# Kernel optimization log

Measured on AMD Instinct MI355X. Metric: run time of the kernel, lower is better.

Reference implementation:

```python
import jax, jax.numpy as jnp
import numpy as np

E = 16      # num experts
K = 2       # top-k
EPS = np.finfo(float).eps


def setup_inputs() -> dict:
    key = jax.random.key(0)
    k1, k2, k3 = jax.random.split(key, 3)
    B, D_IN, D_OUT = 16384, 1024, 512
    x = jax.random.normal(k1, (B, D_IN), dtype=jnp.float32)
    w_router = jax.random.normal(k2, (D_IN, E), dtype=jnp.float32) * 0.02
    w_experts = jax.random.normal(k3, (E, D_IN, D_OUT), dtype=jnp.float32) * 0.02
    return {"x": x, "w_router": w_router, "w_experts": w_experts}


def reference(x, w_router, w_experts):
    # --- noisy_top_k_gating (eval path: clean logits, no noise) ---
    logits = x @ w_router                      # [B, E]
    top_vals, top_idx = jax.lax.top_k(logits, K)   # [B, K]
    top_gates = jax.nn.softmax(top_vals, axis=1)   # softmax over top-k logits
    B = x.shape[0]
    gates = jnp.zeros_like(logits).at[jnp.arange(B)[:, None], top_idx].set(top_gates)  # [B, E]

    # --- per-expert encode (dense form; zero gates null out non-dispatched pairs,
    #     matching SparseDispatcher's sparse dispatch/combine math exactly) ---
    expert_out = jnp.einsum('bd,edh->beh', x, w_experts)  # [B, E, d_out]

    # --- SparseDispatcher.combine: exp -> gate-weight -> index_add -> eps clamp -> log ---
    combined = jnp.einsum('be,beh->bh', gates, jnp.exp(expert_out))  # [B, d_out]
    combined = jnp.where(combined == 0, jnp.asarray(EPS, combined.dtype), combined)
    return jnp.log(combined)
```

## Files before the change

kernel.cpp:

```cpp
#include <hip/hip_runtime.h>
#include <hip/hip_bf16.h>

typedef unsigned short u16_t;
typedef unsigned int   u32_t;

#define B_ROWS  16384
#define D_IN    1024
#define D_OUT   512
#define NEXP    16
#define CNT_STRIDE 16
#define EPSF    2.2204460492503131e-16f

using short8  = __attribute__((ext_vector_type(8))) short;
using floatx4 = __attribute__((ext_vector_type(4))) float;

__device__ __forceinline__ u16_t f2bf(float f) {
    u32_t u = __float_as_uint(f);
    u += 0x7fffu + ((u >> 16) & 1u);
    return (u16_t)(u >> 16);
}

__global__ __launch_bounds__(256) void transpose_wr(
        const float* __restrict__ wr, float* __restrict__ wrT) {
    int i = blockIdx.x * 256 + threadIdx.x;
    int e = i >> 10, d = i & 1023;
    wrT[i] = wr[d * NEXP + e];
}

__global__ __launch_bounds__(256) void convert_x(
        const float* __restrict__ x, u16_t* __restrict__ xb) {
    size_t i = ((size_t)blockIdx.x * 256 + threadIdx.x) * 8;
    float4 a = *(const float4*)(x + i);
    float4 b = *(const float4*)(x + i + 4);
    union { u16_t us[8]; uint4 v; } p;
    p.us[0] = f2bf(a.x); p.us[1] = f2bf(a.y); p.us[2] = f2bf(a.z); p.us[3] = f2bf(a.w);
    p.us[4] = f2bf(b.x); p.us[5] = f2bf(b.y); p.us[6] = f2bf(b.z); p.us[7] = f2bf(b.w);
    *(uint4*)(xb + i) = p.v;
}

__global__ __launch_bounds__(256) void convert_wT(
        const float* __restrict__ w, u16_t* __restrict__ wT) {
    int b = blockIdx.x;
    int e  = b >> 8;
    int k0 = ((b >> 1) & 127) * 8;
    int n  = (b & 1) * 256 + threadIdx.x;
    const float* src = w + ((size_t)e * D_IN + k0) * D_OUT + n;
    union { u16_t us[8]; uint4 v; } p;
    #pragma unroll
    for (int j = 0; j < 8; ++j) p.us[j] = f2bf(src[(size_t)j * D_OUT]);
    *(uint4*)(wT + ((size_t)e * D_OUT + n) * D_IN + k0) = p.v;
}

__global__ __launch_bounds__(256) void router_kernel(
        const float* __restrict__ x, const float* __restrict__ wrT,
        int* __restrict__ counts, int* __restrict__ rowlist,
        float* __restrict__ gatelist) {
    __shared__ float wsh[NEXP * D_IN];
    __shared__ int hist[NEXP], base[NEXP], hist2[NEXP];
    __shared__ unsigned char eidx_sh[32][2];
    __shared__ float g_sh[32][2];

    int t = threadIdx.x;
    {
        const float4* src = (const float4*)wrT;
        float4* dst = (float4*)wsh;
        #pragma unroll
        for (int i = 0; i < 16; ++i) dst[t + 256 * i] = src[t + 256 * i];
    }
    if (t < NEXP) { hist[t] = 0; hist2[t] = 0; }
    __syncthreads();

    int lr = t >> 3, q = t & 7;
    int row = blockIdx.x * 32 + lr;
    const float4* xq = (const float4*)(x + (size_t)row * D_IN + q * 128);

    double acc[NEXP];
    #pragma unroll
    for (int e = 0; e < NEXP; ++e) acc[e] = 0.0;

    for (int i = 0; i < 32; ++i) {
        int ii = (i + q * 4) & 31;
        float4 xv = xq[ii];
        double x0 = xv.x, x1 = xv.y, x2 = xv.z, x3 = xv.w;
        int d = q * 128 + ii * 4;
        #pragma unroll
        for (int e = 0; e < NEXP; ++e) {
            float4 wv = *(const float4*)(&wsh[e * D_IN + d]);
            acc[e] += x0 * (double)wv.x;
            acc[e] += x1 * (double)wv.y;
            acc[e] += x2 * (double)wv.z;
            acc[e] += x3 * (double)wv.w;
        }
    }
    #pragma unroll
    for (int e = 0; e < NEXP; ++e) {
        acc[e] += __shfl_xor(acc[e], 1);
        acc[e] += __shfl_xor(acc[e], 2);
        acc[e] += __shfl_xor(acc[e], 4);
    }
    if (q == 0) {
        int i1 = 0; double v1 = acc[0];
        #pragma unroll
        for (int e = 1; e < NEXP; ++e) if (acc[e] > v1) { v1 = acc[e]; i1 = e; }
        int i2 = -1; double v2 = -1.0e300;
        #pragma unroll
        for (int e = 0; e < NEXP; ++e) if (e != i1 && acc[e] > v2) { v2 = acc[e]; i2 = e; }
        double ed = exp(v2 - v1);
        double s = 1.0 + ed;
        eidx_sh[lr][0] = (unsigned char)i1; g_sh[lr][0] = (float)(1.0 / s);
        eidx_sh[lr][1] = (unsigned char)i2; g_sh[lr][1] = (float)(ed / s);
        atomicAdd(&hist[i1], 1);
        atomicAdd(&hist[i2], 1);
    }
    __syncthreads();
    if (t < NEXP) base[t] = atomicAdd(&counts[t * CNT_STRIDE], hist[t]);
    __syncthreads();
    if (t < 64) {
        int r = t >> 1, sl = t & 1;
        int e = eidx_sh[r][sl];
        int pos = base[e] + atomicAdd(&hist2[e], 1);
        rowlist[e * B_ROWS + pos] = ((blockIdx.x * 32 + r) << 1) | sl;
        gatelist[e * B_ROWS + pos] = g_sh[r][sl];
    }
}

template<bool USE_CONTRIB>
__global__ __launch_bounds__(256) void moe_gemm_bf16(
        const u16_t* __restrict__ xb, const u16_t* __restrict__ wT,
        const int* __restrict__ counts, const int* __restrict__ rowlist,
        const float* __restrict__ gatelist,
        float* __restrict__ out, float* __restrict__ contrib) {
    int e = blockIdx.z;
    int n_e = counts[e * CNT_STRIDE];
    int ty = blockIdx.y;
    if (ty * 128 >= n_e) return;
    int n0 = blockIdx.x * 128;

    __shared__ u16_t Ash[128][40];
    __shared__ u16_t Bsh[128][40];
    __shared__ int   rid_sh[128];
    __shared__ float gt_sh[128];

    int t = threadIdx.x;
    if (t < 128) {
        int gi = ty * 128 + t;
        int v = 0; float g = 0.f;
        if (gi < n_e) { v = rowlist[e * B_ROWS + gi]; g = gatelist[e * B_ROWS + gi]; }
        rid_sh[t] = v; gt_sh[t] = g;
    }
    __syncthreads();

    int hr = t >> 1, hh = t & 1;
    const u16_t* aptr = xb + (size_t)(rid_sh[hr] >> 1) * D_IN + hh * 16;
    const u16_t* bptr = wT + ((size_t)e * D_OUT + n0 + hr) * D_IN + hh * 16;

    int lane = t & 63, wv = t >> 6;
    int wm = wv >> 1, wn = wv & 1;
    int lm = lane & 15, q = lane >> 4;

    floatx4 acc[4][4];
    #pragma unroll
    for (int mi = 0; mi < 4; ++mi)
        #pragma unroll
        for (int ni = 0; ni < 4; ++ni)
            acc[mi][ni] = (floatx4){0.f, 0.f, 0.f, 0.f};

    for (int it = 0; it < D_IN / 32; ++it) {
        uint4 a0 = *(const uint4*)(aptr);
        uint4 a1 = *(const uint4*)(aptr + 8);
        uint4 b0 = *(const uint4*)(bptr);
        uint4 b1 = *(const uint4*)(bptr + 8);
        aptr += 32; bptr += 32;

        __syncthreads();
        *(uint4*)(&Ash[hr][hh * 16])     = a0;
        *(uint4*)(&Ash[hr][hh * 16 + 8]) = a1;
        *(uint4*)(&Bsh[hr][hh * 16])     = b0;
        *(uint4*)(&Bsh[hr][hh * 16 + 8]) = b1;
        __syncthreads();

        short8 afr[4];
        #pragma unroll
        for (int mi = 0; mi < 4; ++mi)
            afr[mi] = *(const short8*)(&Ash[wm * 64 + mi * 16 + lm][q * 8]);
        short8 bfr[4];
        #pragma unroll
        for (int ni = 0; ni < 4; ++ni)
            bfr[ni] = *(const short8*)(&Bsh[wn * 64 + ni * 16 + lm][q * 8]);
        #pragma unroll
        for (int mi = 0; mi < 4; ++mi)
            #pragma unroll
            for (int ni = 0; ni < 4; ++ni)
                acc[mi][ni] = __builtin_amdgcn_mfma_f32_16x16x32_bf16(
                    afr[mi], bfr[ni], acc[mi][ni], 0, 0, 0);
    }

    #pragma unroll
    for (int mi = 0; mi < 4; ++mi) {
        int rbase = wm * 64 + mi * 16 + q * 4;
        #pragma unroll
        for (int r = 0; r < 4; ++r) {
            int row = rbase + r;
            int gi = ty * 128 + row;
            bool ok = gi < n_e;
            int v = rid_sh[row];
            float g = gt_sh[row];
            size_t orow = (size_t)(v >> 1) * D_OUT;
            #pragma unroll
            for (int ni = 0; ni < 4; ++ni) {
                int c = n0 + wn * 64 + ni * 16 + lm;
                float val = g * __expf(acc[mi][ni][r]);
                if (ok) {
                    if (USE_CONTRIB) {
                        float* dst = (v & 1) ? contrib : out;
                        dst[orow + c] = val;
                    } else {
                        atomicAdd(&out[orow + c], val);
                    }
                }
            }
        }
    }
}

template<bool USE_CONTRIB>
__global__ __launch_bounds__(256) void moe_gemm(
        const float* __restrict__ x, const float* __restrict__ w,
        const int* __restrict__ counts, const int* __restrict__ rowlist,
        const float* __restrict__ gatelist,
        float* __restrict__ out, float* __restrict__ contrib) {
    int e = blockIdx.z;
    int n_e = counts[e * CNT_STRIDE];
    int ty = blockIdx.y;
    if (ty * 128 >= n_e) return;
    int n0 = blockIdx.x * 128;

    __shared__ u16_t Ash[128][40];
    __shared__ u32_t Bsh[16][132];
    __shared__ int   rid_sh[128];
    __shared__ float gt_sh[128];

    int t = threadIdx.x;
    if (t < 128) {
        int gi = ty * 128 + t;
        int v = 0; float g = 0.f;
        if (gi < n_e) { v = rowlist[e * B_ROWS + gi]; g = gatelist[e * B_ROWS + gi]; }
        rid_sh[t] = v; gt_sh[t] = g;
    }
    __syncthreads();

    int ar = t >> 1, ah = t & 1;
    const float* xptr = x + (size_t)(rid_sh[ar] >> 1) * D_IN + ah * 16;
    int bkp = t >> 4, bng = t & 15;
    const float* wptr = w + (size_t)e * (D_IN * D_OUT)
                          + (size_t)(2 * bkp) * D_OUT + n0 + bng * 8;

    int lane = t & 63, wv = t >> 6;
    int wm = wv >> 1, wn = wv & 1;
    int lm = lane & 15, q = lane >> 4;

    floatx4 acc[4][4];
    #pragma unroll
    for (int mi = 0; mi < 4; ++mi)
        #pragma unroll
        for (int ni = 0; ni < 4; ++ni)
            acc[mi][ni] = (floatx4){0.f, 0.f, 0.f, 0.f};

    for (int it = 0; it < D_IN / 32; ++it) {
        float4 av0 = *(const float4*)(xptr + 0);
        float4 av1 = *(const float4*)(xptr + 4);
        float4 av2 = *(const float4*)(xptr + 8);
        float4 av3 = *(const float4*)(xptr + 12);
        xptr += 32;
        float4 b0 = *(const float4*)(wptr + 0);
        float4 b1 = *(const float4*)(wptr + 4);
        float4 b2 = *(const float4*)(wptr + D_OUT);
        float4 b3 = *(const float4*)(wptr + D_OUT + 4);
        wptr += 32 * D_OUT;

        __syncthreads();
        {
            union { u16_t us[16]; uint4 v[2]; } ap;
            float af[16] = {av0.x, av0.y, av0.z, av0.w, av1.x, av1.y, av1.z, av1.w,
                            av2.x, av2.y, av2.z, av2.w, av3.x, av3.y, av3.z, av3.w};
            #pragma unroll
            for (int j = 0; j < 16; ++j) ap.us[j] = f2bf(af[j]);
            *(uint4*)(&Ash[ar][ah * 16])     = ap.v[0];
            *(uint4*)(&Ash[ar][ah * 16 + 8]) = ap.v[1];
        }
        {
            union { u32_t up[8]; uint4 v[2]; } bp;
            bp.up[0] = (u32_t)f2bf(b0.x) | ((u32_t)f2bf(b2.x) << 16);
            bp.up[1] = (u32_t)f2bf(b0.y) | ((u32_t)f2bf(b2.y) << 16);
            bp.up[2] = (u32_t)f2bf(b0.z) | ((u32_t)f2bf(b2.z) << 16);
            bp.up[3] = (u32_t)f2bf(b0.w) | ((u32_t)f2bf(b2.w) << 16);
            bp.up[4] = (u32_t)f2bf(b1.x) | ((u32_t)f2bf(b3.x) << 16);
            bp.up[5] = (u32_t)f2bf(b1.y) | ((u32_t)f2bf(b3.y) << 16);
            bp.up[6] = (u32_t)f2bf(b1.z) | ((u32_t)f2bf(b3.z) << 16);
            bp.up[7] = (u32_t)f2bf(b1.w) | ((u32_t)f2bf(b3.w) << 16);
            *(uint4*)(&Bsh[bkp][bng * 8])     = bp.v[0];
            *(uint4*)(&Bsh[bkp][bng * 8 + 4]) = bp.v[1];
        }
        __syncthreads();

        short8 afr[4];
        #pragma unroll
        for (int mi = 0; mi < 4; ++mi)
            afr[mi] = *(const short8*)(&Ash[wm * 64 + mi * 16 + lm][q * 8]);
        short8 bfr[4];
        #pragma unroll
        for (int ni = 0; ni < 4; ++ni) {
            int nn = wn * 64 + ni * 16 + lm;
            union { uint4 u; short8 s; } cv;
            cv.u.x = Bsh[q * 4 + 0][nn];
            cv.u.y = Bsh[q * 4 + 1][nn];
            cv.u.z = Bsh[q * 4 + 2][nn];
            cv.u.w = Bsh[q * 4 + 3][nn];
            bfr[ni] = cv.s;
        }
        #pragma unroll
        for (int mi = 0; mi < 4; ++mi)
            #pragma unroll
            for (int ni = 0; ni < 4; ++ni)
                acc[mi][ni] = __builtin_amdgcn_mfma_f32_16x16x32_bf16(
                    afr[mi], bfr[ni], acc[mi][ni], 0, 0, 0);
    }

    #pragma unroll
    for (int mi = 0; mi < 4; ++mi) {
        int rbase = wm * 64 + mi * 16 + q * 4;
        #pragma unroll
        for (int r = 0; r < 4; ++r) {
            int row = rbase + r;
            int gi = ty * 128 + row;
            bool ok = gi < n_e;
            int v = rid_sh[row];
            float g = gt_sh[row];
            size_t orow = (size_t)(v >> 1) * D_OUT;
            #pragma unroll
            for (int ni = 0; ni < 4; ++ni) {
                int c = n0 + wn * 64 + ni * 16 + lm;
                float val = g * __expf(acc[mi][ni][r]);
                if (ok) {
                    if (USE_CONTRIB) {
                        float* dst = (v & 1) ? contrib : out;
                        dst[orow + c] = val;
                    } else {
                        atomicAdd(&out[orow + c], val);
                    }
                }
            }
        }
    }
}

__global__ __launch_bounds__(256) void combine_add_log(
        float* __restrict__ out, const float* __restrict__ contrib, int n4) {
    int i = blockIdx.x * blockDim.x + threadIdx.x;
    if (i >= n4) return;
    float4 a = ((const float4*)out)[i];
    float4 b = ((const float4*)contrib)[i];
    float4 r;
    float s;
    s = a.x + b.x; s = (s == 0.f) ? EPSF : s; r.x = __logf(s);
    s = a.y + b.y; s = (s == 0.f) ? EPSF : s; r.y = __logf(s);
    s = a.z + b.z; s = (s == 0.f) ? EPSF : s; r.z = __logf(s);
    s = a.w + b.w; s = (s == 0.f) ? EPSF : s; r.w = __logf(s);
    ((float4*)out)[i] = r;
}

__global__ __launch_bounds__(256) void log_inplace(float* __restrict__ out, int n4) {
    int i = blockIdx.x * blockDim.x + threadIdx.x;
    if (i >= n4) return;
    float4 a = ((float4*)out)[i];
    float4 r;
    float s;
    s = a.x; s = (s == 0.f) ? EPSF : s; r.x = __logf(s);
    s = a.y; s = (s == 0.f) ? EPSF : s; r.y = __logf(s);
    s = a.z; s = (s == 0.f) ? EPSF : s; r.z = __logf(s);
    s = a.w; s = (s == 0.f) ? EPSF : s; r.w = __logf(s);
    ((float4*)out)[i] = r;
}

extern "C" void kernel_launch(void* const* d_in, const int* in_sizes, int n_in,
                              void* d_out, int out_size, void* d_ws, size_t ws_size,
                              hipStream_t stream) {
    const float* x  = (const float*)d_in[0];
    const float* wr = (const float*)d_in[1];
    const float* we = (const float*)d_in[2];
    float* out = (float*)d_out;
    char* ws = (char*)d_ws;

    size_t off = 0;
    int*   counts  = (int*)(ws + off);   off += 1024;
    int*   rowlist = (int*)(ws + off);   off += (size_t)NEXP * B_ROWS * 4;
    float* gates   = (float*)(ws + off); off += (size_t)NEXP * B_ROWS * 4;
    float* wrT     = (float*)(ws + off); off += (size_t)NEXP * D_IN * 4;
    float* contrib = (float*)(ws + off); off += (size_t)B_ROWS * D_OUT * 4;
    size_t tier2_need = off;
    u16_t* xb      = (u16_t*)(ws + off); off += (size_t)B_ROWS * D_IN * 2;
    u16_t* wTb     = (u16_t*)(ws + off); off += (size_t)NEXP * D_IN * D_OUT * 2;
    size_t tier3_need = off;

    hipMemsetAsync(counts, 0, 1024, stream);
    transpose_wr<<<NEXP * D_IN / 256, 256, 0, stream>>>(wr, wrT);
    router_kernel<<<B_ROWS / 32, 256, 0, stream>>>(x, wrT, counts, rowlist, gates);

    dim3 g(D_OUT / 128, B_ROWS / 128, NEXP);
    int n4 = B_ROWS * D_OUT / 4;

    if (ws_size >= tier3_need) {
        convert_x<<<(B_ROWS * D_IN / 8) / 256, 256, 0, stream>>>(x, xb);
        convert_wT<<<NEXP * 128 * 2, 256, 0, stream>>>(we, wTb);
        moe_gemm_bf16<true><<<g, 256, 0, stream>>>(xb, wTb, counts, rowlist, gates, out, contrib);
        combine_add_log<<<(n4 + 255) / 256, 256, 0, stream>>>(out, contrib, n4);
    } else if (ws_size >= tier2_need) {
        moe_gemm<true><<<g, 256, 0, stream>>>(x, we, counts, rowlist, gates, out, contrib);
        combine_add_log<<<(n4 + 255) / 256, 256, 0, stream>>>(out, contrib, n4);
    } else {
        hipMemsetAsync(out, 0, (size_t)B_ROWS * D_OUT * 4, stream);
        moe_gemm<false><<<g, 256, 0, stream>>>(x, we, counts, rowlist, gates, out, nullptr);
        log_inplace<<<(n4 + 255) / 256, 256, 0, stream>>>(out, n4);
    }
}
```

Measured before the change: 272.5 us.

## Use direct global-to-LDS loads in MoE GEMM, tile weight transpose, coalesce router

The bf16 MoE GEMM now stages A and B tiles with global_load_lds (16-byte direct global-to-LDS copies) into a fragment-ordered LDS layout, so the register round trip and padded-array indexing go away. The weight convert/transpose kernel now goes through a shared-memory tile, so both its fp32 reads and its bf16 writes are coalesced. The router reads x in an interleaved order so adjacent threads touch adjacent float4s. The GEMM loop is still single-buffered with two barriers per step, and the direct-LDS path relies on the exact per-lane address layout.

```diff
diff --git a/kernel.cpp b/kernel.cpp
--- a/kernel.cpp
+++ b/kernel.cpp
@@ -13,6 +13,10 @@
 
 using short8  = __attribute__((ext_vector_type(8))) short;
 using floatx4 = __attribute__((ext_vector_type(4))) float;
+
+#define GLDS16(gp, lp) __builtin_amdgcn_global_load_lds( \
+    (const __attribute__((address_space(1))) void*)(gp), \
+    (__attribute__((address_space(3))) void*)(lp), 16, 0, 0)
 
 __device__ __forceinline__ u16_t f2bf(float f) {
     u32_t u = __float_as_uint(f);
@@ -40,15 +44,29 @@
 
 __global__ __launch_bounds__(256) void convert_wT(
         const float* __restrict__ w, u16_t* __restrict__ wT) {
-    int b = blockIdx.x;
-    int e  = b >> 8;
-    int k0 = ((b >> 1) & 127) * 8;
-    int n  = (b & 1) * 256 + threadIdx.x;
-    const float* src = w + ((size_t)e * D_IN + k0) * D_OUT + n;
-    union { u16_t us[8]; uint4 v; } p;
-    #pragma unroll
-    for (int j = 0; j < 8; ++j) p.us[j] = f2bf(src[(size_t)j * D_OUT]);
-    *(uint4*)(wT + ((size_t)e * D_OUT + n) * D_IN + k0) = p.v;
+    __shared__ u16_t sh[128][72];
+    int e = blockIdx.z, k0 = blockIdx.x * 128, n0 = blockIdx.y * 64;
+    int t = threadIdx.x;
+    int kk = t >> 4, nc = (t & 15) * 4;
+    const float* src = w + ((size_t)e * D_IN + k0 + kk) * D_OUT + n0 + nc;
+    #pragma unroll
+    for (int p = 0; p < 8; ++p) {
+        float4 v = *(const float4*)(src + (size_t)p * 16 * D_OUT);
+        sh[p * 16 + kk][nc + 0] = f2bf(v.x);
+        sh[p * 16 + kk][nc + 1] = f2bf(v.y);
+        sh[p * 16 + kk][nc + 2] = f2bf(v.z);
+        sh[p * 16 + kk][nc + 3] = f2bf(v.w);
+    }
+    __syncthreads();
+    int nn = t >> 2, c = t & 3;
+    u16_t* dst = wT + ((size_t)e * D_OUT + n0 + nn) * D_IN + k0 + c * 32;
+    #pragma unroll
+    for (int j = 0; j < 4; ++j) {
+        union { u16_t us[8]; uint4 v; } p;
+        #pragma unroll
+        for (int jj = 0; jj < 8; ++jj) p.us[jj] = sh[c * 32 + j * 8 + jj][nn];
+        *(uint4*)(dst + j * 8) = p.v;
+    }
 }
 
 __global__ __launch_bounds__(256) void router_kernel(
@@ -72,20 +90,18 @@
 
     int lr = t >> 3, q = t & 7;
     int row = blockIdx.x * 32 + lr;
-    const float4* xq = (const float4*)(x + (size_t)row * D_IN + q * 128);
+    const float4* xq = (const float4*)(x + (size_t)row * D_IN);
 
     double acc[NEXP];
     #pragma unroll
     for (int e = 0; e < NEXP; ++e) acc[e] = 0.0;
 
     for (int i = 0; i < 32; ++i) {
-        int ii = (i + q * 4) & 31;
-        float4 xv = xq[ii];
+        float4 xv = xq[i * 8 + q];
         double x0 = xv.x, x1 = xv.y, x2 = xv.z, x3 = xv.w;
-        int d = q * 128 + ii * 4;
         #pragma unroll
         for (int e = 0; e < NEXP; ++e) {
-            float4 wv = *(const float4*)(&wsh[e * D_IN + d]);
+            float4 wv = *(const float4*)(&wsh[e * D_IN + i * 32 + q * 4]);
             acc[e] += x0 * (double)wv.x;
             acc[e] += x1 * (double)wv.y;
             acc[e] += x2 * (double)wv.z;
@@ -136,8 +152,8 @@
     if (ty * 128 >= n_e) return;
     int n0 = blockIdx.x * 128;
 
-    __shared__ u16_t Ash[128][40];
-    __shared__ u16_t Bsh[128][40];
+    __shared__ __align__(16) u16_t Af[8192];
+    __shared__ __align__(16) u16_t Bf[8192];
     __shared__ int   rid_sh[128];
     __shared__ float gt_sh[128];
 
@@ -150,14 +166,20 @@
     }
     __syncthreads();
 
-    int hr = t >> 1, hh = t & 1;
-    const u16_t* aptr = xb + (size_t)(rid_sh[hr] >> 1) * D_IN + hh * 16;
-    const u16_t* bptr = wT + ((size_t)e * D_OUT + n0 + hr) * D_IN + hh * 16;
-
     int lane = t & 63, wv = t >> 6;
     int wm = wv >> 1, wn = wv & 1;
     int lm = lane & 15, q = lane >> 4;
 
+    int m0 = 2 * wv, m1 = 2 * wv + 1;
+    const u16_t* aG0 = xb + (size_t)(rid_sh[m0 * 16 + lm] >> 1) * D_IN + q * 8;
+    const u16_t* aG1 = xb + (size_t)(rid_sh[m1 * 16 + lm] >> 1) * D_IN + q * 8;
+    const u16_t* bG0 = wT + ((size_t)e * D_OUT + n0 + m0 * 16 + lm) * D_IN + q * 8;
+    const u16_t* bG1 = wT + ((size_t)e * D_OUT + n0 + m1 * 16 + lm) * D_IN + q * 8;
+    u16_t* aL0 = Af + m0 * 512;
+    u16_t* aL1 = Af + m1 * 512;
+    u16_t* bL0 = Bf + m0 * 512;
+    u16_t* bL1 = Bf + m1 * 512;
+
     floatx4 acc[4][4];
     #pragma unroll
     for (int mi = 0; mi < 4; ++mi)
@@ -166,27 +188,21 @@
             acc[mi][ni] = (floatx4){0.f, 0.f, 0.f, 0.f};
 
     for (int it = 0; it < D_IN / 32; ++it) {
-        uint4 a0 = *(const uint4*)(aptr);
-        uint4 a1 = *(const uint4*)(aptr + 8);
-        uint4 b0 = *(const uint4*)(bptr);
-        uint4 b1 = *(const uint4*)(bptr + 8);
-        aptr += 32; bptr += 32;
-
         __syncthreads();
-        *(uint4*)(&Ash[hr][hh * 16])     = a0;
-        *(uint4*)(&Ash[hr][hh * 16 + 8]) = a1;
-        *(uint4*)(&Bsh[hr][hh * 16])     = b0;
-        *(uint4*)(&Bsh[hr][hh * 16 + 8]) = b1;
+        GLDS16(aG0, aL0);
+        GLDS16(aG1, aL1);
+        GLDS16(bG0, bL0);
+        GLDS16(bG1, bL1);
+        aG0 += 32; aG1 += 32; bG0 += 32; bG1 += 32;
         __syncthreads();
 
-        short8 afr[4];
+        short8 afr[4], bfr[4];
         #pragma unroll
         for (int mi = 0; mi < 4; ++mi)
-            afr[mi] = *(const short8*)(&Ash[wm * 64 + mi * 16 + lm][q * 8]);
-        short8 bfr[4];
+            afr[mi] = *(const short8*)(Af + (wm * 4 + mi) * 512 + lane * 8);
         #pragma unroll
         for (int ni = 0; ni < 4; ++ni)
-            bfr[ni] = *(const short8*)(&Bsh[wn * 64 + ni * 16 + lm][q * 8]);
+            bfr[ni] = *(const short8*)(Bf + (wn * 4 + ni) * 512 + lane * 8);
         #pragma unroll
         for (int mi = 0; mi < 4; ++mi)
             #pragma unroll
@@ -411,7 +427,8 @@
 
     if (ws_size >= tier3_need) {
         convert_x<<<(B_ROWS * D_IN / 8) / 256, 256, 0, stream>>>(x, xb);
-        convert_wT<<<NEXP * 128 * 2, 256, 0, stream>>>(we, wTb);
+        dim3 gw(D_IN / 128, D_OUT / 64, NEXP);
+        convert_wT<<<gw, 256, 0, stream>>>(we, wTb);
         moe_gemm_bf16<true><<<g, 256, 0, stream>>>(xb, wTb, counts, rowlist, gates, out, contrib);
         combine_add_log<<<(n4 + 255) / 256, 256, 0, stream>>>(out, contrib, n4);
     } else if (ws_size >= tier2_need) {
```

Measured after the change: 287.3 us. 5.4% more time.
